# Kernel tuning notes

Hardware: AMD Instinct MI355X
Metric: run time of the kernel (lower is better)

Reference implementation:

```python
import jax, jax.numpy as jnp
import numpy as np

SEQ, B, IN, H, OUT = 600, 4096, 6, 30, 61


def setup_inputs() -> dict:
    key = jax.random.key(0)
    ks = jax.random.split(key, 9)
    s_ih = 1.0 / np.sqrt(H)
    return {
        "X": jax.random.normal(ks[0], (SEQ, B, IN), dtype=jnp.float32),
        "W_ih": jax.random.uniform(ks[1], (4 * H, IN), jnp.float32, -s_ih, s_ih),
        "W_hh": jax.random.uniform(ks[2], (4 * H, H), jnp.float32, -s_ih, s_ih),
        "b_ih": jax.random.uniform(ks[3], (4 * H,), jnp.float32, -s_ih, s_ih),
        "b_hh": jax.random.uniform(ks[4], (4 * H,), jnp.float32, -s_ih, s_ih),
        "W1": jax.random.uniform(ks[5], (H, H), jnp.float32, -s_ih, s_ih),
        "b1": jax.random.uniform(ks[6], (H,), jnp.float32, -s_ih, s_ih),
        "W2": jax.random.uniform(ks[7], (OUT, H), jnp.float32, -s_ih, s_ih),
        "b2": jax.random.uniform(ks[8], (OUT,), jnp.float32, -s_ih, s_ih),
        "batch_size": B,
    }


def _lstm_last_h(X, W_ih, W_hh, b_ih, b_hh):
    # Precompute input projections for all timesteps: [T, B, 4H]
    xg = jnp.einsum("tbi,gi->tbg", X, W_ih) + b_ih + b_hh
    h0 = jnp.zeros((X.shape[1], W_hh.shape[1]), X.dtype)
    c0 = jnp.zeros_like(h0)

    def step(carry, xg_t):
        h, c = carry
        g = xg_t + h @ W_hh.T  # [B, 4H]
        i, f, gg, o = jnp.split(g, 4, axis=-1)  # PyTorch gate order i,f,g,o
        c = jax.nn.sigmoid(f) * c + jax.nn.sigmoid(i) * jnp.tanh(gg)
        h = jax.nn.sigmoid(o) * jnp.tanh(c)
        return (h, c), None

    (h, _), _ = jax.lax.scan(step, (h0, c0), xg)
    return h  # out[-1, :, :]


def reference(X, W_ih, W_hh, b_ih, b_hh, W1, b1, W2, b2, batch_size):
    h = _lstm_last_h(X, W_ih, W_hh, b_ih, b_hh)
    out = h @ W1.T + b1  # fc1
    # dropout(p=0.6) is identity in eval mode
    out = out @ W2.T + b2  # fc2
    return out  # [B, 61]
```

## Files before the change

kernel.cpp:

```cpp
#include <hip/hip_runtime.h>


#define SEQ   600
#define BATCH 4096
#define INP   6
#define HID   30
#define NOUT  61
#define EPB   8

__device__ __forceinline__ float rcp_(float x) { return __builtin_amdgcn_rcpf(x); }
__device__ __forceinline__ float sigm_(float x) { return rcp_(1.0f + __expf(-x)); }
__device__ __forceinline__ float tanh_(float x) {
    float e = __expf(2.0f * x);
    return 1.0f - 2.0f * rcp_(e + 1.0f);
}

extern "C" __global__ void __launch_bounds__(256, 2)
lstm_fused(const float* __restrict__ X,   const float* __restrict__ Wih,
           const float* __restrict__ Whh, const float* __restrict__ bih,
           const float* __restrict__ bhh, const float* __restrict__ W1,
           const float* __restrict__ b1,  const float* __restrict__ W2,
           const float* __restrict__ b2,  float* __restrict__ out)
{
    __shared__ float h_sh[EPB][32];
    __shared__ float o1_sh[EPB][32];

    const int tid  = threadIdx.x;
    const int u    = tid & 31;
    const int e    = tid >> 5;
    const int b    = blockIdx.x * EPB + e;
    const bool act = (u < HID);

    h_sh[e][u] = 0.0f;

    float wi[32], wf[32], wg[32], wo[32];
    float vi[INP], vf[INP], vg[INP], vo[INP];
    float bi = 0.f, bf = 0.f, bg = 0.f, bo = 0.f;
    #pragma unroll
    for (int k = 0; k < 32; ++k) { wi[k] = 0.f; wf[k] = 0.f; wg[k] = 0.f; wo[k] = 0.f; }
    #pragma unroll
    for (int k = 0; k < INP; ++k) { vi[k] = 0.f; vf[k] = 0.f; vg[k] = 0.f; vo[k] = 0.f; }

    if (act) {
        #pragma unroll
        for (int k = 0; k < HID; ++k) {
            wi[k] = Whh[(0 * HID + u) * HID + k];
            wf[k] = Whh[(1 * HID + u) * HID + k];
            wg[k] = Whh[(2 * HID + u) * HID + k];
            wo[k] = Whh[(3 * HID + u) * HID + k];
        }
        #pragma unroll
        for (int k = 0; k < INP; ++k) {
            vi[k] = Wih[(0 * HID + u) * INP + k];
            vf[k] = Wih[(1 * HID + u) * INP + k];
            vg[k] = Wih[(2 * HID + u) * INP + k];
            vo[k] = Wih[(3 * HID + u) * INP + k];
        }
        bi = bih[0 * HID + u] + bhh[0 * HID + u];
        bf = bih[1 * HID + u] + bhh[1 * HID + u];
        bg = bih[2 * HID + u] + bhh[2 * HID + u];
        bo = bih[3 * HID + u] + bhh[3 * HID + u];
    }

    float c = 0.f, h = 0.f;
    float x[INP], xn[INP] = {};
    {
        const float* p = X + (size_t)b * INP;
        #pragma unroll
        for (int k = 0; k < INP; ++k) x[k] = p[k];
    }
    asm volatile("s_waitcnt lgkmcnt(0)" ::: "memory");

    const float4* h4p = (const float4*)(&h_sh[e][0]);

    for (int t = 0; t < SEQ; ++t) {
        if (t + 1 < SEQ) {
            const float* p = X + ((size_t)(t + 1) * BATCH + b) * INP;
            #pragma unroll
            for (int k = 0; k < INP; ++k) xn[k] = p[k];
        }

        float ai = bi, af = bf, ag = bg, ao = bo;
        #pragma unroll
        for (int k = 0; k < INP; ++k) {
            ai = fmaf(vi[k], x[k], ai);
            af = fmaf(vf[k], x[k], af);
            ag = fmaf(vg[k], x[k], ag);
            ao = fmaf(vo[k], x[k], ao);
        }
        #pragma unroll
        for (int q = 0; q < 8; ++q) {
            float4 hv = h4p[q];
            ai = fmaf(wi[4*q+0], hv.x, ai); af = fmaf(wf[4*q+0], hv.x, af);
            ag = fmaf(wg[4*q+0], hv.x, ag); ao = fmaf(wo[4*q+0], hv.x, ao);
            ai = fmaf(wi[4*q+1], hv.y, ai); af = fmaf(wf[4*q+1], hv.y, af);
            ag = fmaf(wg[4*q+1], hv.y, ag); ao = fmaf(wo[4*q+1], hv.y, ao);
            ai = fmaf(wi[4*q+2], hv.z, ai); af = fmaf(wf[4*q+2], hv.z, af);
            ag = fmaf(wg[4*q+2], hv.z, ag); ao = fmaf(wo[4*q+2], hv.z, ao);
            ai = fmaf(wi[4*q+3], hv.w, ai); af = fmaf(wf[4*q+3], hv.w, af);
            ag = fmaf(wg[4*q+3], hv.w, ag); ao = fmaf(wo[4*q+3], hv.w, ao);
        }

        float gi = sigm_(ai);
        float gf = sigm_(af);
        float go = sigm_(ao);
        float gg = tanh_(ag);
        c = gf * c + gi * gg;
        h = go * tanh_(c);

        h_sh[e][u] = h;
        asm volatile("s_waitcnt lgkmcnt(0)" ::: "memory");

        #pragma unroll
        for (int k = 0; k < INP; ++k) x[k] = xn[k];
    }

    if (act) {
        float a1 = b1[u];
        const float* w1r = W1 + u * HID;
        #pragma unroll
        for (int k = 0; k < HID; ++k) a1 = fmaf(w1r[k], h_sh[e][k], a1);
        o1_sh[e][u] = a1;
    }
    asm volatile("s_waitcnt lgkmcnt(0)" ::: "memory");

    if (act) {
        for (int o = u; o < NOUT; o += HID) {
            float a2 = b2[o];
            const float* w2r = W2 + o * HID;
            #pragma unroll
            for (int k = 0; k < HID; ++k) a2 = fmaf(w2r[k], o1_sh[e][k], a2);
            out[(size_t)b * NOUT + o] = a2;
        }
    }
}

extern "C" void kernel_launch(void* const* d_in, const int* in_sizes, int n_in,
                              void* d_out, int out_size, void* d_ws, size_t ws_size,
                              hipStream_t stream) {
    const float* X   = (const float*)d_in[0];
    const float* Wih = (const float*)d_in[1];
    const float* Whh = (const float*)d_in[2];
    const float* bih = (const float*)d_in[3];
    const float* bhh = (const float*)d_in[4];
    const float* W1  = (const float*)d_in[5];
    const float* b1  = (const float*)d_in[6];
    const float* W2  = (const float*)d_in[7];
    const float* b2  = (const float*)d_in[8];
    float* out = (float*)d_out;

    dim3 grid(BATCH / EPB);
    dim3 block(256);
    hipLaunchKernelGGL(lstm_fused, grid, block, 0, stream,
                       X, Wih, Whh, bih, bhh, W1, b1, W2, b2, out);
}
```

Before: 360.3 us.

## Split LSTM gates across wave halves with packed FMA and shuffle exchange

Each batch element now gets a full 64-lane wave instead of a 32-lane half-wave. Each half computes two of the four gates (i/g or f/o) using packed two-wide float FMAs, and the gate values are swapped between halves with a cross-lane shuffle. The aim is to halve the per-thread recurrent FMA chain and register use, which allows higher occupancy (launch bounds of 4). In exchange it doubles the thread count per element, adds a shuffle on the critical step path, and moves the exponentials to exp2 with folded constants.

```diff
diff --git a/kernel.cpp b/kernel.cpp
--- a/kernel.cpp
+++ b/kernel.cpp
@@ -6,132 +6,136 @@
 #define INP   6
 #define HID   30
 #define NOUT  61
-#define EPB   8
+#define EPW   1
+#define WPB   4
+
+typedef float f32x2 __attribute__((ext_vector_type(2)));
 
 __device__ __forceinline__ float rcp_(float x) { return __builtin_amdgcn_rcpf(x); }
-__device__ __forceinline__ float sigm_(float x) { return rcp_(1.0f + __expf(-x)); }
-__device__ __forceinline__ float tanh_(float x) {
-    float e = __expf(2.0f * x);
-    return 1.0f - 2.0f * rcp_(e + 1.0f);
-}
+__device__ __forceinline__ float exp2_(float x) { return __builtin_amdgcn_exp2f(x); }
 
-extern "C" __global__ void __launch_bounds__(256, 2)
-lstm_fused(const float* __restrict__ X,   const float* __restrict__ Wih,
-           const float* __restrict__ Whh, const float* __restrict__ bih,
-           const float* __restrict__ bhh, const float* __restrict__ W1,
-           const float* __restrict__ b1,  const float* __restrict__ W2,
-           const float* __restrict__ b2,  float* __restrict__ out)
+extern "C" __global__ void __launch_bounds__(256, 4)
+lstm_fused2(const float* __restrict__ X,   const float* __restrict__ Wih,
+            const float* __restrict__ Whh, const float* __restrict__ bih,
+            const float* __restrict__ bhh, const float* __restrict__ W1,
+            const float* __restrict__ b1,  const float* __restrict__ W2,
+            const float* __restrict__ b2,  float* __restrict__ out)
 {
-    __shared__ float h_sh[EPB][32];
-    __shared__ float o1_sh[EPB][32];
+    __shared__ float h_sh[WPB][32];
+    __shared__ float o1_sh[WPB][32];
 
     const int tid  = threadIdx.x;
-    const int u    = tid & 31;
-    const int e    = tid >> 5;
-    const int b    = blockIdx.x * EPB + e;
+    const int lane = tid & 63;
+    const int u    = lane & 31;
+    const int half = lane >> 5;
+    const int e    = __builtin_amdgcn_readfirstlane(tid >> 6);
+    const int b    = blockIdx.x * WPB + e;
     const bool act = (u < HID);
 
-    h_sh[e][u] = 0.0f;
+    if (lane < 32) h_sh[e][lane] = 0.0f;
 
-    float wi[32], wf[32], wg[32], wo[32];
-    float vi[INP], vf[INP], vg[INP], vo[INP];
-    float bi = 0.f, bf = 0.f, bg = 0.f, bo = 0.f;
+    const int rowA = (half * 2 + 0) * HID + u;
+    const int rowB = (half * 2 + 1) * HID + u;
+
+    f32x2 wA[16], wB[16];
+    f32x2 xA[3], xB[3];
+    float bA = 0.f, bB = 0.f;
     #pragma unroll
-    for (int k = 0; k < 32; ++k) { wi[k] = 0.f; wf[k] = 0.f; wg[k] = 0.f; wo[k] = 0.f; }
+    for (int j = 0; j < 16; ++j) { wA[j] = (f32x2)0.f; wB[j] = (f32x2)0.f; }
     #pragma unroll
-    for (int k = 0; k < INP; ++k) { vi[k] = 0.f; vf[k] = 0.f; vg[k] = 0.f; vo[k] = 0.f; }
+    for (int j = 0; j < 3; ++j) { xA[j] = (f32x2)0.f; xB[j] = (f32x2)0.f; }
 
     if (act) {
+        const float* ra = Whh + rowA * HID;
+        const float* rb = Whh + rowB * HID;
         #pragma unroll
-        for (int k = 0; k < HID; ++k) {
-            wi[k] = Whh[(0 * HID + u) * HID + k];
-            wf[k] = Whh[(1 * HID + u) * HID + k];
-            wg[k] = Whh[(2 * HID + u) * HID + k];
-            wo[k] = Whh[(3 * HID + u) * HID + k];
+        for (int j = 0; j < 15; ++j) {
+            wA[j] = f32x2{ra[2*j], ra[2*j+1]};
+            wB[j] = f32x2{rb[2*j], rb[2*j+1]};
         }
+        const float* va = Wih + rowA * INP;
+        const float* vb = Wih + rowB * INP;
         #pragma unroll
-        for (int k = 0; k < INP; ++k) {
-            vi[k] = Wih[(0 * HID + u) * INP + k];
-            vf[k] = Wih[(1 * HID + u) * INP + k];
-            vg[k] = Wih[(2 * HID + u) * INP + k];
-            vo[k] = Wih[(3 * HID + u) * INP + k];
+        for (int j = 0; j < 3; ++j) {
+            xA[j] = f32x2{va[2*j], va[2*j+1]};
+            xB[j] = f32x2{vb[2*j], vb[2*j+1]};
         }
-        bi = bih[0 * HID + u] + bhh[0 * HID + u];
-        bf = bih[1 * HID + u] + bhh[1 * HID + u];
-        bg = bih[2 * HID + u] + bhh[2 * HID + u];
-        bo = bih[3 * HID + u] + bhh[3 * HID + u];
+        bA = bih[rowA] + bhh[rowA];
+        bB = bih[rowB] + bhh[rowB];
     }
 
+    const float mA = half ? -2.8853900818f : -1.4426950409f;
+    const float sA = half ? 2.0f : 1.0f;
+    const float cA = half ? -1.0f : 0.0f;
+
     float c = 0.f, h = 0.f;
-    float x[INP], xn[INP] = {};
+    f32x2 x2[3], xn2[3];
     {
-        const float* p = X + (size_t)b * INP;
+        const f32x2* p = (const f32x2*)(X + (size_t)b * INP);
         #pragma unroll
-        for (int k = 0; k < INP; ++k) x[k] = p[k];
+        for (int j = 0; j < 3; ++j) x2[j] = p[j];
     }
     asm volatile("s_waitcnt lgkmcnt(0)" ::: "memory");
 
-    const float4* h4p = (const float4*)(&h_sh[e][0]);
+    const f32x2* h2 = (const f32x2*)(&h_sh[e][0]);
 
     for (int t = 0; t < SEQ; ++t) {
         if (t + 1 < SEQ) {
-            const float* p = X + ((size_t)(t + 1) * BATCH + b) * INP;
+            const f32x2* p = (const f32x2*)(X + ((size_t)(t + 1) * BATCH + b) * INP);
             #pragma unroll
-            for (int k = 0; k < INP; ++k) xn[k] = p[k];
+            for (int j = 0; j < 3; ++j) xn2[j] = p[j];
         }
 
-        float ai = bi, af = bf, ag = bg, ao = bo;
+        f32x2 accA = f32x2{bA, 0.f};
+        f32x2 accB = f32x2{bB, 0.f};
         #pragma unroll
-        for (int k = 0; k < INP; ++k) {
-            ai = fmaf(vi[k], x[k], ai);
-            af = fmaf(vf[k], x[k], af);
-            ag = fmaf(vg[k], x[k], ag);
-            ao = fmaf(vo[k], x[k], ao);
+        for (int j = 0; j < 16; ++j) {
+            f32x2 hv = h2[j];
+            accA = __builtin_elementwise_fma(wA[j], hv, accA);
+            accB = __builtin_elementwise_fma(wB[j], hv, accB);
         }
         #pragma unroll
-        for (int q = 0; q < 8; ++q) {
-            float4 hv = h4p[q];
-            ai = fmaf(wi[4*q+0], hv.x, ai); af = fmaf(wf[4*q+0], hv.x, af);
-            ag = fmaf(wg[4*q+0], hv.x, ag); ao = fmaf(wo[4*q+0], hv.x, ao);
-            ai = fmaf(wi[4*q+1], hv.y, ai); af = fmaf(wf[4*q+1], hv.y, af);
-            ag = fmaf(wg[4*q+1], hv.y, ag); ao = fmaf(wo[4*q+1], hv.y, ao);
-            ai = fmaf(wi[4*q+2], hv.z, ai); af = fmaf(wf[4*q+2], hv.z, af);
-            ag = fmaf(wg[4*q+2], hv.z, ag); ao = fmaf(wo[4*q+2], hv.z, ao);
-            ai = fmaf(wi[4*q+3], hv.w, ai); af = fmaf(wf[4*q+3], hv.w, af);
-            ag = fmaf(wg[4*q+3], hv.w, ag); ao = fmaf(wo[4*q+3], hv.w, ao);
+        for (int j = 0; j < 3; ++j) {
+            accA = __builtin_elementwise_fma(xA[j], x2[j], accA);
+            accB = __builtin_elementwise_fma(xB[j], x2[j], accB);
         }
+        const float aA = accA.x + accA.y;
+        const float aB = accB.x + accB.y;
 
-        float gi = sigm_(ai);
-        float gf = sigm_(af);
-        float go = sigm_(ao);
-        float gg = tanh_(ag);
-        c = gf * c + gi * gg;
-        h = go * tanh_(c);
+        const float nA = fmaf(sA, rcp_(1.0f + exp2_(mA * aA)), cA);
+        const float nB = rcp_(1.0f + exp2_(-1.4426950409f * aB));
 
-        h_sh[e][u] = h;
+        const float vA = __shfl_xor(nA, 32);
+        const float vB = __shfl_xor(nB, 32);
+
+        const float F = half ? vB : nB;
+        const float O = half ? nB : vB;
+        c = fmaf(F, c, nA * vA);
+        const float tc = 1.0f - 2.0f * rcp_(exp2_(2.8853900818f * c) + 1.0f);
+        h = O * tc;
+
+        if (lane < HID) h_sh[e][lane] = h;
         asm volatile("s_waitcnt lgkmcnt(0)" ::: "memory");
 
         #pragma unroll
-        for (int k = 0; k < INP; ++k) x[k] = xn[k];
+        for (int j = 0; j < 3; ++j) x2[j] = xn2[j];
     }
 
-    if (act) {
-        float a1 = b1[u];
-        const float* w1r = W1 + u * HID;
+    if (lane < HID) {
+        float a1 = b1[lane];
+        const float* w1r = W1 + lane * HID;
         #pragma unroll
         for (int k = 0; k < HID; ++k) a1 = fmaf(w1r[k], h_sh[e][k], a1);
-        o1_sh[e][u] = a1;
+        o1_sh[e][lane] = a1;
     }
     asm volatile("s_waitcnt lgkmcnt(0)" ::: "memory");
 
-    if (act) {
-        for (int o = u; o < NOUT; o += HID) {
-            float a2 = b2[o];
-            const float* w2r = W2 + o * HID;
-            #pragma unroll
-            for (int k = 0; k < HID; ++k) a2 = fmaf(w2r[k], o1_sh[e][k], a2);
-            out[(size_t)b * NOUT + o] = a2;
-        }
+    if (lane < NOUT) {
+        float a2 = b2[lane];
+        const float* w2r = W2 + lane * HID;
+        #pragma unroll
+        for (int k = 0; k < HID; ++k) a2 = fmaf(w2r[k], o1_sh[e][k], a2);
+        out[(size_t)b * NOUT + lane] = a2;
     }
 }
 
@@ -149,8 +153,8 @@
     const float* b2  = (const float*)d_in[8];
     float* out = (float*)d_out;
 
-    dim3 grid(BATCH / EPB);
-    dim3 block(256);
-    hipLaunchKernelGGL(lstm_fused, grid, block, 0, stream,
+    dim3 grid(BATCH / WPB);
+    dim3 block(64 * WPB);
+    hipLaunchKernelGGL(lstm_fused2, grid, block, 0, stream,
                        X, Wih, Whh, bih, bhh, W1, b1, W2, b2, out);
 }
```

New measurement: 464.0 us. +28.8%, slower.

## Use packed FMA for gate dot products and shrink blocks to one wavefront

Applied to the files above, without the earlier changes.

Rewrites the recurrent gate matvec to use two-wide packed FMAs (v_pk_fma) with even/odd accumulators, loading weights as dwordx2 via inline asm, and uses exp2 intrinsics for sigmoid/tanh. Blocks shrink from 256 threads (8 sequences) to 64 threads (2 sequences, one wavefront), giving 2048 blocks. The aim is to halve FMA issue count on the serial per-timestep critical path and spread work across more CUs. It risks extra register pressure and lower per-CU occupancy from the small blocks.

```diff
diff --git a/kernel.cpp b/kernel.cpp
--- a/kernel.cpp
+++ b/kernel.cpp
@@ -6,121 +6,158 @@
 #define INP   6
 #define HID   30
 #define NOUT  61
-#define EPB   8
 
-__device__ __forceinline__ float rcp_(float x) { return __builtin_amdgcn_rcpf(x); }
-__device__ __forceinline__ float sigm_(float x) { return rcp_(1.0f + __expf(-x)); }
-__device__ __forceinline__ float tanh_(float x) {
-    float e = __expf(2.0f * x);
-    return 1.0f - 2.0f * rcp_(e + 1.0f);
-}
+typedef float f32x2 __attribute__((ext_vector_type(2)));
 
-extern "C" __global__ void __launch_bounds__(256, 2)
-lstm_fused(const float* __restrict__ X,   const float* __restrict__ Wih,
-           const float* __restrict__ Whh, const float* __restrict__ bih,
-           const float* __restrict__ bhh, const float* __restrict__ W1,
-           const float* __restrict__ b1,  const float* __restrict__ W2,
-           const float* __restrict__ b2,  float* __restrict__ out)
+__device__ __forceinline__ float rcp_(float x)  { return __builtin_amdgcn_rcpf(x); }
+__device__ __forceinline__ float exp2_(float x) { return __builtin_amdgcn_exp2f(x); }
+#define LOG2E  1.4426950408889634f
+#define LOG2E2 2.8853900817779268f
+
+extern "C" __global__ void __launch_bounds__(64, 2)
+lstm_fused4(const float* __restrict__ X,   const float* __restrict__ Wih,
+            const float* __restrict__ Whh, const float* __restrict__ bih,
+            const float* __restrict__ bhh, const float* __restrict__ W1,
+            const float* __restrict__ b1,  const float* __restrict__ W2,
+            const float* __restrict__ b2,  float* __restrict__ out)
 {
-    __shared__ float h_sh[EPB][32];
-    __shared__ float o1_sh[EPB][32];
+    __shared__ float h_sh[2][32];
+    __shared__ float o1_sh[2][32];
 
-    const int tid  = threadIdx.x;
-    const int u    = tid & 31;
-    const int e    = tid >> 5;
-    const int b    = blockIdx.x * EPB + e;
+    const int lane = threadIdx.x;
+    const int half = lane >> 5;
+    const int u    = lane & 31;
+    const int uu   = (u < HID) ? u : (HID - 1);
+    const int b    = blockIdx.x * 2 + half;
     const bool act = (u < HID);
 
-    h_sh[e][u] = 0.0f;
+    h_sh[half][u] = 0.0f;
 
-    float wi[32], wf[32], wg[32], wo[32];
-    float vi[INP], vf[INP], vg[INP], vo[INP];
-    float bi = 0.f, bf = 0.f, bg = 0.f, bo = 0.f;
+    const float* r0 = Whh + (0 * HID + uu) * HID;
+    const float* r1 = Whh + (1 * HID + uu) * HID;
+    const float* r2 = Whh + (2 * HID + uu) * HID;
+    const float* r3 = Whh + (3 * HID + uu) * HID;
+
+    f32x2 w0[15], w1[15], w2[15], w3[15];
     #pragma unroll
-    for (int k = 0; k < 32; ++k) { wi[k] = 0.f; wf[k] = 0.f; wg[k] = 0.f; wo[k] = 0.f; }
+    for (int j = 0; j < 15; ++j) {
+        asm volatile("global_load_dwordx2 %0, %1, off" : "=v"(w0[j]) : "v"(r0 + 2 * j));
+        asm volatile("global_load_dwordx2 %0, %1, off" : "=v"(w1[j]) : "v"(r1 + 2 * j));
+        asm volatile("global_load_dwordx2 %0, %1, off" : "=v"(w2[j]) : "v"(r2 + 2 * j));
+        asm volatile("global_load_dwordx2 %0, %1, off" : "=v"(w3[j]) : "v"(r3 + 2 * j));
+    }
+    const float* s0 = Wih + (0 * HID + uu) * INP;
+    const float* s1 = Wih + (1 * HID + uu) * INP;
+    const float* s2 = Wih + (2 * HID + uu) * INP;
+    const float* s3 = Wih + (3 * HID + uu) * INP;
+
+    f32x2 xw0[3], xw1[3], xw2[3], xw3[3];
     #pragma unroll
-    for (int k = 0; k < INP; ++k) { vi[k] = 0.f; vf[k] = 0.f; vg[k] = 0.f; vo[k] = 0.f; }
+    for (int j = 0; j < 3; ++j) {
+        asm volatile("global_load_dwordx2 %0, %1, off" : "=v"(xw0[j]) : "v"(s0 + 2 * j));
+        asm volatile("global_load_dwordx2 %0, %1, off" : "=v"(xw1[j]) : "v"(s1 + 2 * j));
+        asm volatile("global_load_dwordx2 %0, %1, off" : "=v"(xw2[j]) : "v"(s2 + 2 * j));
+        asm volatile("global_load_dwordx2 %0, %1, off" : "=v"(xw3[j]) : "v"(s3 + 2 * j));
+    }
+    asm volatile("s_waitcnt vmcnt(0)" ::: "memory");
 
+    float bb0 = 0.f, bb1 = 0.f, bb2 = 0.f, bb3 = 0.f;
     if (act) {
-        #pragma unroll
-        for (int k = 0; k < HID; ++k) {
-            wi[k] = Whh[(0 * HID + u) * HID + k];
-            wf[k] = Whh[(1 * HID + u) * HID + k];
-            wg[k] = Whh[(2 * HID + u) * HID + k];
-            wo[k] = Whh[(3 * HID + u) * HID + k];
-        }
-        #pragma unroll
-        for (int k = 0; k < INP; ++k) {
-            vi[k] = Wih[(0 * HID + u) * INP + k];
-            vf[k] = Wih[(1 * HID + u) * INP + k];
-            vg[k] = Wih[(2 * HID + u) * INP + k];
-            vo[k] = Wih[(3 * HID + u) * INP + k];
-        }
-        bi = bih[0 * HID + u] + bhh[0 * HID + u];
-        bf = bih[1 * HID + u] + bhh[1 * HID + u];
-        bg = bih[2 * HID + u] + bhh[2 * HID + u];
-        bo = bih[3 * HID + u] + bhh[3 * HID + u];
+        bb0 = bih[0 * HID + u] + bhh[0 * HID + u];
+        bb1 = bih[1 * HID + u] + bhh[1 * HID + u];
+        bb2 = bih[2 * HID + u] + bhh[2 * HID + u];
+        bb3 = bih[3 * HID + u] + bhh[3 * HID + u];
     }
+    asm volatile("" : "+v"(bb0), "+v"(bb1), "+v"(bb2), "+v"(bb3));
 
     float c = 0.f, h = 0.f;
-    float x[INP], xn[INP] = {};
+
+    f32x2 xc0, xc1, xc2, xn0, xn1, xn2;
     {
-        const float* p = X + (size_t)b * INP;
-        #pragma unroll
-        for (int k = 0; k < INP; ++k) x[k] = p[k];
+        const f32x2* p = (const f32x2*)(X + (size_t)b * INP);
+        xc0 = p[0]; xc1 = p[1]; xc2 = p[2];
     }
     asm volatile("s_waitcnt lgkmcnt(0)" ::: "memory");
 
-    const float4* h4p = (const float4*)(&h_sh[e][0]);
+    const float4* h4p = (const float4*)(&h_sh[half][0]);
+    const f32x2*  h2p = (const f32x2*)(&h_sh[half][0]);
 
     for (int t = 0; t < SEQ; ++t) {
-        if (t + 1 < SEQ) {
-            const float* p = X + ((size_t)(t + 1) * BATCH + b) * INP;
-            #pragma unroll
-            for (int k = 0; k < INP; ++k) xn[k] = p[k];
+        const int tn = (t + 1 < SEQ) ? (t + 1) : (SEQ - 1);
+        const f32x2* p = (const f32x2*)(X + ((size_t)tn * BATCH + b) * INP);
+        xn0 = p[0]; xn1 = p[1]; xn2 = p[2];
+
+        float4 H0 = h4p[0], H1 = h4p[1], H2 = h4p[2], H3 = h4p[3];
+        float4 H4 = h4p[4], H5 = h4p[5], H6 = h4p[6];
+        f32x2  Ht = h2p[14];
+
+        f32x2 a0e = f32x2{bb0, 0.f}, a0o = (f32x2)0.f;
+        f32x2 a1e = f32x2{bb1, 0.f}, a1o = (f32x2)0.f;
+        f32x2 a2e = f32x2{bb2, 0.f}, a2o = (f32x2)0.f;
+        f32x2 a3e = f32x2{bb3, 0.f}, a3o = (f32x2)0.f;
+
+        #define PK4(J, HX, HY, E)  do {                                   \
+            f32x2 hv = f32x2{HX, HY};                                     \
+            a0##E = __builtin_elementwise_fma(w0[J], hv, a0##E);          \
+            a1##E = __builtin_elementwise_fma(w1[J], hv, a1##E);          \
+            a2##E = __builtin_elementwise_fma(w2[J], hv, a2##E);          \
+            a3##E = __builtin_elementwise_fma(w3[J], hv, a3##E);          \
+        } while (0)
+        PK4(0,  H0.x, H0.y, e); PK4(1,  H0.z, H0.w, o);
+        PK4(2,  H1.x, H1.y, e); PK4(3,  H1.z, H1.w, o);
+        PK4(4,  H2.x, H2.y, e); PK4(5,  H2.z, H2.w, o);
+        PK4(6,  H3.x, H3.y, e); PK4(7,  H3.z, H3.w, o);
+        PK4(8,  H4.x, H4.y, e); PK4(9,  H4.z, H4.w, o);
+        PK4(10, H5.x, H5.y, e); PK4(11, H5.z, H5.w, o);
+        PK4(12, H6.x, H6.y, e); PK4(13, H6.z, H6.w, o);
+        {
+            a0e = __builtin_elementwise_fma(w0[14], Ht, a0e);
+            a1e = __builtin_elementwise_fma(w1[14], Ht, a1e);
+            a2e = __builtin_elementwise_fma(w2[14], Ht, a2e);
+            a3e = __builtin_elementwise_fma(w3[14], Ht, a3e);
         }
+        #undef PK4
+        a0o = __builtin_elementwise_fma(xw0[0], xc0, a0o);
+        a1o = __builtin_elementwise_fma(xw1[0], xc0, a1o);
+        a2o = __builtin_elementwise_fma(xw2[0], xc0, a2o);
+        a3o = __builtin_elementwise_fma(xw3[0], xc0, a3o);
+        a0e = __builtin_elementwise_fma(xw0[1], xc1, a0e);
+        a1e = __builtin_elementwise_fma(xw1[1], xc1, a1e);
+        a2e = __builtin_elementwise_fma(xw2[1], xc1, a2e);
+        a3e = __builtin_elementwise_fma(xw3[1], xc1, a3e);
+        a0o = __builtin_elementwise_fma(xw0[2], xc2, a0o);
+        a1o = __builtin_elementwise_fma(xw1[2], xc2, a1o);
+        a2o = __builtin_elementwise_fma(xw2[2], xc2, a2o);
+        a3o = __builtin_elementwise_fma(xw3[2], xc2, a3o);
 
-        float ai = bi, af = bf, ag = bg, ao = bo;
-        #pragma unroll
-        for (int k = 0; k < INP; ++k) {
-            ai = fmaf(vi[k], x[k], ai);
-            af = fmaf(vf[k], x[k], af);
-            ag = fmaf(vg[k], x[k], ag);
-            ao = fmaf(vo[k], x[k], ao);
-        }
-        #pragma unroll
-        for (int q = 0; q < 8; ++q) {
-            float4 hv = h4p[q];
-            ai = fmaf(wi[4*q+0], hv.x, ai); af = fmaf(wf[4*q+0], hv.x, af);
-            ag = fmaf(wg[4*q+0], hv.x, ag); ao = fmaf(wo[4*q+0], hv.x, ao);
-            ai = fmaf(wi[4*q+1], hv.y, ai); af = fmaf(wf[4*q+1], hv.y, af);
-            ag = fmaf(wg[4*q+1], hv.y, ag); ao = fmaf(wo[4*q+1], hv.y, ao);
-            ai = fmaf(wi[4*q+2], hv.z, ai); af = fmaf(wf[4*q+2], hv.z, af);
-            ag = fmaf(wg[4*q+2], hv.z, ag); ao = fmaf(wo[4*q+2], hv.z, ao);
-            ai = fmaf(wi[4*q+3], hv.w, ai); af = fmaf(wf[4*q+3], hv.w, af);
-            ag = fmaf(wg[4*q+3], hv.w, ag); ao = fmaf(wo[4*q+3], hv.w, ao);
-        }
+        const f32x2 g0v = a0e + a0o, g1v = a1e + a1o;
+        const f32x2 g2v = a2e + a2o, g3v = a3e + a3o;
+        const float g0 = g0v.x + g0v.y;
+        const float g1 = g1v.x + g1v.y;
+        const float g2 = g2v.x + g2v.y;
+        const float g3 = g3v.x + g3v.y;
 
-        float gi = sigm_(ai);
-        float gf = sigm_(af);
-        float go = sigm_(ao);
-        float gg = tanh_(ag);
-        c = gf * c + gi * gg;
-        h = go * tanh_(c);
+        const float si = rcp_(1.0f + exp2_(-LOG2E * g0));
+        const float sf = rcp_(1.0f + exp2_(-LOG2E * g1));
+        const float tg = 1.0f - 2.0f * rcp_(exp2_(LOG2E2 * g2) + 1.0f);
+        const float so = rcp_(1.0f + exp2_(-LOG2E * g3));
 
-        h_sh[e][u] = h;
+        c = fmaf(sf, c, si * tg);
+        const float tc = 1.0f - 2.0f * rcp_(exp2_(LOG2E2 * c) + 1.0f);
+        h = so * tc;
+
+        if (act) h_sh[half][u] = h;
         asm volatile("s_waitcnt lgkmcnt(0)" ::: "memory");
 
-        #pragma unroll
-        for (int k = 0; k < INP; ++k) x[k] = xn[k];
+        xc0 = xn0; xc1 = xn1; xc2 = xn2;
     }
 
     if (act) {
         float a1 = b1[u];
         const float* w1r = W1 + u * HID;
         #pragma unroll
-        for (int k = 0; k < HID; ++k) a1 = fmaf(w1r[k], h_sh[e][k], a1);
-        o1_sh[e][u] = a1;
+        for (int k = 0; k < HID; ++k) a1 = fmaf(w1r[k], h_sh[half][k], a1);
+        o1_sh[half][u] = a1;
     }
     asm volatile("s_waitcnt lgkmcnt(0)" ::: "memory");
 
@@ -129,7 +166,7 @@
             float a2 = b2[o];
             const float* w2r = W2 + o * HID;
             #pragma unroll
-            for (int k = 0; k < HID; ++k) a2 = fmaf(w2r[k], o1_sh[e][k], a2);
+            for (int k = 0; k < HID; ++k) a2 = fmaf(w2r[k], o1_sh[half][k], a2);
             out[(size_t)b * NOUT + o] = a2;
         }
     }
@@ -149,8 +186,8 @@
     const float* b2  = (const float*)d_in[8];
     float* out = (float*)d_out;
 
-    dim3 grid(BATCH / EPB);
-    dim3 block(256);
-    hipLaunchKernelGGL(lstm_fused, grid, block, 0, stream,
+    dim3 grid(BATCH / 2);
+    dim3 block(64);
+    hipLaunchKernelGGL(lstm_fused4, grid, block, 0, stream,
                        X, Wih, Whh, bih, bhh, W1, b1, W2, b2, out);
 }
```

New measurement: 350.2 us. -2.8%, faster.
